# Optimization experiments

Measured on AMD Instinct MI355X. Metric: run time of the kernel, lower is better.

Reference implementation:

```python
import jax, jax.numpy as jnp
import numpy as np

N_NODES = 50000
N_EDGES = 800000
N_GRAPHS = 512
IN_DIM = 50
H = 128  # hidden_channels


def _init_linear(key, out_dim, in_dim, bias=True):
    k1, k2 = jax.random.split(key)
    bound = 1.0 / np.sqrt(in_dim)
    W = jax.random.uniform(k1, (out_dim, in_dim), jnp.float32, -bound, bound)
    if bias:
        b = jax.random.uniform(k2, (out_dim,), jnp.float32, -bound, bound)
        return W, b
    return W


def setup_inputs() -> dict:
    key = jax.random.key(0)
    ks = jax.random.split(key, 16)
    x = jax.random.normal(ks[0], (N_NODES, IN_DIM), jnp.float32)
    edge_index = jax.random.randint(ks[1], (2, N_EDGES), 0, N_NODES, jnp.int64)
    batch = jnp.sort(jax.random.randint(ks[2], (N_NODES,), 0, N_GRAPHS, jnp.int64))
    Wl1, bl1 = _init_linear(ks[3], H, IN_DIM)
    Wr1 = _init_linear(ks[4], H, IN_DIM, bias=False)
    Wl2, bl2 = _init_linear(ks[5], 2 * H, H)
    Wr2 = _init_linear(ks[6], 2 * H, H, bias=False)
    Wl3, bl3 = _init_linear(ks[7], 4 * H, 2 * H)
    Wr3 = _init_linear(ks[8], 4 * H, 2 * H, bias=False)
    Wf1, bf1 = _init_linear(ks[9], 2 * H, 4 * H)
    Wf2, bf2 = _init_linear(ks[10], H, 2 * H)
    Wo, bo = _init_linear(ks[11], 1, H)
    return dict(x=x, edge_index=edge_index, batch=batch,
                Wl1=Wl1, bl1=bl1, Wr1=Wr1,
                Wl2=Wl2, bl2=bl2, Wr2=Wr2,
                Wl3=Wl3, bl3=bl3, Wr3=Wr3,
                Wf1=Wf1, bf1=bf1, Wf2=Wf2, bf2=bf2, Wo=Wo, bo=bo)


def sage_conv(x, src, dst, deg_inv, Wl, bl, Wr):
    # mean-aggregate neighbor features at destination nodes, then linear
    agg = jax.ops.segment_sum(x[src], dst, num_segments=N_NODES) * deg_inv
    return agg @ Wl.T + bl + x @ Wr.T


def reference(x, edge_index, batch, Wl1, bl1, Wr1, Wl2, bl2, Wr2,
              Wl3, bl3, Wr3, Wf1, bf1, Wf2, bf2, Wo, bo):
    src, dst = edge_index[0], edge_index[1]
    deg = jax.ops.segment_sum(jnp.ones((N_EDGES,), x.dtype), dst, num_segments=N_NODES)
    deg_inv = (1.0 / jnp.maximum(deg, 1.0))[:, None]

    x1 = jax.nn.leaky_relu(sage_conv(x, src, dst, deg_inv, Wl1, bl1, Wr1))
    x2 = jax.nn.relu(sage_conv(x1, src, dst, deg_inv, Wl2, bl2, Wr2))
    x3 = jax.nn.relu(sage_conv(x2, src, dst, deg_inv, Wl3, bl3, Wr3))

    # global mean pool per graph
    pool_sum = jax.ops.segment_sum(x3, batch, num_segments=N_GRAPHS)
    cnt = jax.ops.segment_sum(jnp.ones((N_NODES,), x.dtype), batch, num_segments=N_GRAPHS)
    x_pool = pool_sum / jnp.maximum(cnt, 1.0)[:, None]

    x4 = jax.nn.relu(x_pool @ Wf1.T + bf1)
    x5 = jax.nn.relu(x4 @ Wf2.T + bf2)
    return jax.nn.sigmoid(x5 @ Wo.T + bo)
```

## Files before the change

### kernel.cpp

```cpp
#include <hip/hip_runtime.h>
#include <math.h>

#define N_NODES 50000
#define N_EDGES 800000
#define N_GRAPHS 512
#define M_PAD 50176
#define SEG_SZ 6250
#define EPT 8
#define SEG_BLOCKS 391
#define CAP 64

typedef unsigned char u8;
typedef unsigned short u16;
typedef unsigned int u32;
typedef long i64;
using floatx4 = __attribute__((ext_vector_type(4))) float;
using floatx2 = __attribute__((ext_vector_type(2))) float;

__device__ __forceinline__ u8 f2fp8(float v) {
    return (u8)(__builtin_amdgcn_cvt_pk_fp8_f32(v, v, 0, false) & 0xFF);
}
__device__ __forceinline__ u32 pack4fp8(float a, float b, float c, float d) {
    u32 p = __builtin_amdgcn_cvt_pk_fp8_f32(a, b, 0, false);
    return __builtin_amdgcn_cvt_pk_fp8_f32(c, d, p, true);
}
__device__ __forceinline__ void acc16fp8(float* acc, uint4 u) {
    const u32 w[4] = {u.x, u.y, u.z, u.w};
    #pragma unroll
    for (int j = 0; j < 4; ++j) {
        floatx2 lo = __builtin_amdgcn_cvt_pk_f32_fp8((int)w[j], false);
        floatx2 hi = __builtin_amdgcn_cvt_pk_f32_fp8((int)w[j], true);
        acc[j * 4 + 0] += lo[0]; acc[j * 4 + 1] += lo[1];
        acc[j * 4 + 2] += hi[0]; acc[j * 4 + 3] += hi[1];
    }
}

__device__ __forceinline__ void load_lds16(const u8* g, u8* l) {
    __builtin_amdgcn_global_load_lds(
        (const __attribute__((address_space(1))) u32*)g,
        (__attribute__((address_space(3))) u32*)l, 16, 0, 0);
}
template<int N> __device__ __forceinline__ void waitcnt_vm() {
    __builtin_amdgcn_s_waitcnt(0x0F70 | N);
}
__device__ __forceinline__ void raw_barrier() {
    asm volatile("s_barrier" ::: "memory");
}

__global__ __launch_bounds__(256) void prep_kernel(
    const int* __restrict__ batch, int* __restrict__ gstart,
    const float* __restrict__ x,
    const float* __restrict__ Wl1, const float* __restrict__ Wr1,
    const float* __restrict__ Wl2, const float* __restrict__ Wr2,
    const float* __restrict__ Wl3, const float* __restrict__ Wr3,
    const float* __restrict__ Wf1, const float* __restrict__ Wf2,
    u8* __restrict__ abuf1,
    u8* __restrict__ wb1, u8* __restrict__ wb2, u8* __restrict__ wb3,
    float* __restrict__ Wf1T, float* __restrict__ Wf2T)
{
    if (blockIdx.x < 196) {
        int i = blockIdx.x * 256 + threadIdx.x;
        if (i >= N_NODES) return;
        int b = batch[i];
        int bp = (i == 0) ? -1 : batch[i - 1];
        for (int g = bp + 1; g <= b; ++g) gstart[g] = i;
        if (i == N_NODES - 1)
            for (int g = b + 1; g <= N_GRAPHS; ++g) gstart[g] = N_NODES;
        return;
    }
    int i = (blockIdx.x - 196) * 256 + threadIdx.x;
    if (i < N_NODES * 16) {
        int n = i >> 4, c = (i & 15) * 4;
        float v[4];
        #pragma unroll
        for (int j = 0; j < 4; ++j) {
            int cc = c + j;
            v[j] = (cc < 50) ? x[n * 50 + cc] : 0.0f;
        }
        *(u32*)(abuf1 + (size_t)n * 128 + 64 + c) = pack4fp8(v[0], v[1], v[2], v[3]);
        return;
    }
    i -= N_NODES * 16;
    if (i < 128 * 64) {
        int o = i / 64, c = i % 64;
        float vl = (c < 50) ? Wl1[o * 50 + c] : 0.0f;
        float vr = (c < 50) ? Wr1[o * 50 + c] : 0.0f;
        wb1[(size_t)o * 128 + c] = f2fp8(vl);
        wb1[(size_t)o * 128 + 64 + c] = f2fp8(vr);
        return;
    }
    i -= 128 * 64;
    if (i < 256 * 128) {
        int o = i / 128, c = i % 128;
        wb2[(size_t)o * 256 + c] = f2fp8(Wl2[o * 128 + c]);
        wb2[(size_t)o * 256 + 128 + c] = f2fp8(Wr2[o * 128 + c]);
        return;
    }
    i -= 256 * 128;
    if (i < 512 * 256) {
        int o = i / 256, c = i % 256;
        wb3[(size_t)o * 512 + c] = f2fp8(Wl3[o * 256 + c]);
        wb3[(size_t)o * 512 + 256 + c] = f2fp8(Wr3[o * 256 + c]);
        return;
    }
    i -= 512 * 256;
    if (i < 256 * 512) {
        int o = i >> 9, k = i & 511;
        Wf1T[(size_t)k * 256 + o] = Wf1[(size_t)o * 512 + k];
        return;
    }
    i -= 256 * 512;
    if (i < 128 * 256) {
        int o = i >> 8, k = i & 255;
        Wf2T[(size_t)k * 128 + o] = Wf2[(size_t)o * 256 + k];
    }
}

__global__ __launch_bounds__(256) void fill_seg_kernel(const int* __restrict__ src,
                                                       const int* __restrict__ dst,
                                                       int* __restrict__ cursor,
                                                       u16* __restrict__ csr) {
    const int seg = blockIdx.x & 7;
    const int lo = seg * SEG_SZ, hi = lo + SEG_SZ;
    int e = (blockIdx.x >> 3) * (256 * EPT) + threadIdx.x;
    #pragma unroll
    for (int j = 0; j < EPT; ++j, e += 256) {
        if (e < N_EDGES) {
            int d = dst[e];
            if (d >= lo && d < hi) {
                int p = atomicAdd(&cursor[d], 1);
                csr[d * CAP + p] = (u16)src[e];
            }
        }
    }
}

template<int DINP>
__global__ __launch_bounds__(256) void csr_agg_kernel(const int* __restrict__ cnt,
                                                      const u16* __restrict__ csr,
                                                      u8* __restrict__ abuf) {
    constexpr int STRIDE = 2 * DINP;
    constexpr int LPR = DINP / 16;
    constexpr int EPW = 64 / LPR;
    const int wave = threadIdx.x >> 6, lane = threadIdx.x & 63;
    const int n = blockIdx.x * 4 + wave;
    if (n >= N_NODES) return;
    const int sub = lane / LPR;
    const int li = lane % LPR;
    const int deg = cnt[n];
    const int s0 = n * CAP, s1 = s0 + deg;

    float acc[16] = {};
    const u8* xin = abuf + DINP;

    int e = s0 + sub;
    for (; e + EPW < s1; e += 2 * EPW) {
        int i0 = csr[e], i1 = csr[e + EPW];
        uint4 u0 = *(const uint4*)(xin + (size_t)i0 * STRIDE + li * 16);
        uint4 u1 = *(const uint4*)(xin + (size_t)i1 * STRIDE + li * 16);
        acc16fp8(acc, u0);
        acc16fp8(acc, u1);
    }
    for (; e < s1; e += EPW) {
        int i0 = csr[e];
        uint4 u0 = *(const uint4*)(xin + (size_t)i0 * STRIDE + li * 16);
        acc16fp8(acc, u0);
    }

    #pragma unroll
    for (int off = 32; off >= LPR; off >>= 1) {
        #pragma unroll
        for (int c = 0; c < 16; ++c) acc[c] += __shfl_down(acc[c], off);
    }

    if (lane < LPR) {
        float sc = 1.0f / fmaxf((float)deg, 1.0f);
        uint4 o;
        o.x = pack4fp8(acc[0] * sc, acc[1] * sc, acc[2] * sc, acc[3] * sc);
        o.y = pack4fp8(acc[4] * sc, acc[5] * sc, acc[6] * sc, acc[7] * sc);
        o.z = pack4fp8(acc[8] * sc, acc[9] * sc, acc[10] * sc, acc[11] * sc);
        o.w = pack4fp8(acc[12] * sc, acc[13] * sc, acc[14] * sc, acc[15] * sc);
        *(uint4*)(abuf + (size_t)n * STRIDE + li * 16) = o;
    }
}

template<int K, int NB, int ACT>
__global__ __launch_bounds__(256) void gemm_fp8_kernel(
    const u8* __restrict__ A, const u8* __restrict__ W,
    const float* __restrict__ bias,
    u8* __restrict__ out8, int gstride, int goff, int N)
{
    constexpr int NKB = K / 32;
    constexpr int MT = M_PAD / 128;
    constexpr int MCHUNK = MT / 8;
    __shared__ __align__(16) u8 As[3][128 * 32];
    __shared__ __align__(16) u8 Bs[3][128 * 32];

    const int bx = blockIdx.x;
    const int xcd = bx & 7;
    const int seq = bx >> 3;
    const int n = seq % NB;
    const int m = xcd * MCHUNK + seq / NB;
    if (m >= MT) return;
    const int bm = m * 128;
    const int bn = n * 128;

    const int tid = threadIdx.x;
    const int wave = tid >> 6, lane = tid & 63;
    const int wm = (wave & 1) * 64, wn = (wave >> 1) * 64;
    const int lm = lane & 15, lq = lane >> 4;

    const int srow = wave * 32 + (lane >> 1);
    const int scol = ((lane & 1) ^ ((lane >> 3) & 1)) * 16;
    const u8* gA = A + (size_t)(bm + srow) * K + scol;
    const u8* gB = W + (size_t)(bn + srow) * K + scol;
    const int lbase = wave * 32 * 32;

    auto stage = [&](int s, int r) {
        const int ko = s * 32;
        load_lds16(gA + ko, &As[r][lbase]);
        load_lds16(gB + ko, &Bs[r][lbase]);
    };

    floatx4 acc[4][4] = {};

    stage(0, 0);
    stage(1, 1);

    const int csw = (((lq >> 1) ^ ((lm >> 2) & 1)) << 4) + (lq & 1) * 8;

    #pragma unroll
    for (int kb = 0; kb < NKB; ++kb) {
        if (kb + 2 < NKB) stage(kb + 2, (kb + 2) % 3);
        const int rem = NKB - 1 - kb;
        if (rem >= 2)      waitcnt_vm<4>();
        else if (rem == 1) waitcnt_vm<2>();
        else               waitcnt_vm<0>();
        raw_barrier();

        const int r = kb % 3;
        i64 af[4], bfr[4];
        #pragma unroll
        for (int mi = 0; mi < 4; ++mi)
            af[mi] = *(const i64*)&As[r][(wm + mi * 16 + lm) * 32 + csw];
        #pragma unroll
        for (int ni = 0; ni < 4; ++ni)
            bfr[ni] = *(const i64*)&Bs[r][(wn + ni * 16 + lm) * 32 + csw];
        #pragma unroll
        for (int mi = 0; mi < 4; ++mi)
            #pragma unroll
            for (int ni = 0; ni < 4; ++ni)
                acc[mi][ni] = __builtin_amdgcn_mfma_f32_16x16x32_fp8_fp8(
                    af[mi], bfr[ni], acc[mi][ni], 0, 0, 0);
        raw_barrier();
    }

    #pragma unroll
    for (int mi = 0; mi < 4; ++mi) {
        int node0 = bm + wm + mi * 16 + lq * 4;
        #pragma unroll
        for (int ni = 0; ni < 4; ++ni) {
            int o = bn + wn + ni * 16 + lm;
            float bi = bias[o];
            #pragma unroll
            for (int r = 0; r < 4; ++r) {
                int node = node0 + r;
                if (node >= N) continue;
                float v = acc[mi][ni][r] + bi;
                if (ACT == 0) v = (v > 0.0f) ? v : 0.01f * v;
                else          v = fmaxf(v, 0.0f);
                out8[(size_t)node * gstride + goff + o] = f2fp8(v);
            }
        }
    }
}

template<int K, int NB, int ACT>
__global__ __launch_bounds__(256) void gemm64_fp8_kernel(
    const u8* __restrict__ A, const u8* __restrict__ W,
    const float* __restrict__ bias,
    u8* __restrict__ out8, int gstride, int goff, int N)
{
    constexpr int NKB = K / 64;
    constexpr int MT = M_PAD / 128;
    constexpr int MCHUNK = MT / 8;
    __shared__ __align__(16) u8 As[3][128 * 64];
    __shared__ __align__(16) u8 Bs[3][128 * 64];

    const int bx = blockIdx.x;
    const int xcd = bx & 7;
    const int seq = bx >> 3;
    const int n = seq % NB;
    const int m = xcd * MCHUNK + seq / NB;
    if (m >= MT) return;
    const int bm = m * 128;
    const int bn = n * 128;

    const int tid = threadIdx.x;
    const int wave = tid >> 6, lane = tid & 63;
    const int wm = (wave & 1) * 64, wn = (wave >> 1) * 64;
    const int lm = lane & 15, lq = lane >> 4;

    const int srow = wave * 16 + (lane >> 2);
    const int scd  = ((lane & 3) ^ ((srow >> 1) & 3)) << 4;
    const u8* gA = A + (size_t)(bm + srow) * K + scd;
    const u8* gB = W + (size_t)(bn + srow) * K + scd;
    const int lbase = wave * 1024;

    auto stage = [&](int s, int r) {
        const int ko = s * 64;
        load_lds16(gA + ko,                    &As[r][lbase]);
        load_lds16(gA + (size_t)64 * K + ko,   &As[r][lbase + 4096]);
        load_lds16(gB + ko,                    &Bs[r][lbase]);
        load_lds16(gB + (size_t)64 * K + ko,   &Bs[r][lbase + 4096]);
    };

    floatx4 acc[4][4] = {};

    stage(0, 0);
    stage(1, 1);

    const int pr = (lm >> 1) & 3;
    const int c0 = (((lq >> 1) ^ pr) << 4)       + ((lq & 1) << 3);
    const int c1 = (((2 + (lq >> 1)) ^ pr) << 4) + ((lq & 1) << 3);

    #pragma unroll
    for (int kb = 0; kb < NKB; ++kb) {
        if (kb + 2 < NKB) stage(kb + 2, (kb + 2) % 3);
        const int rem = NKB - 1 - kb;
        if (rem >= 2)      waitcnt_vm<8>();
        else if (rem == 1) waitcnt_vm<4>();
        else               waitcnt_vm<0>();
        raw_barrier();

        const int r = kb % 3;
        i64 af[4][2], bfr[4][2];
        #pragma unroll
        for (int mi = 0; mi < 4; ++mi) {
            const int base = (wm + mi * 16 + lm) * 64;
            af[mi][0] = *(const i64*)&As[r][base + c0];
            af[mi][1] = *(const i64*)&As[r][base + c1];
        }
        #pragma unroll
        for (int ni = 0; ni < 4; ++ni) {
            const int base = (wn + ni * 16 + lm) * 64;
            bfr[ni][0] = *(const i64*)&Bs[r][base + c0];
            bfr[ni][1] = *(const i64*)&Bs[r][base + c1];
        }
        #pragma unroll
        for (int mi = 0; mi < 4; ++mi)
            #pragma unroll
            for (int ni = 0; ni < 4; ++ni) {
                acc[mi][ni] = __builtin_amdgcn_mfma_f32_16x16x32_fp8_fp8(
                    af[mi][0], bfr[ni][0], acc[mi][ni], 0, 0, 0);
                acc[mi][ni] = __builtin_amdgcn_mfma_f32_16x16x32_fp8_fp8(
                    af[mi][1], bfr[ni][1], acc[mi][ni], 0, 0, 0);
            }
        raw_barrier();
    }

    #pragma unroll
    for (int mi = 0; mi < 4; ++mi) {
        int node0 = bm + wm + mi * 16 + lq * 4;
        #pragma unroll
        for (int ni = 0; ni < 4; ++ni) {
            int o = bn + wn + ni * 16 + lm;
            float bi = bias[o];
            #pragma unroll
            for (int r = 0; r < 4; ++r) {
                int node = node0 + r;
                if (node >= N) continue;
                float v = acc[mi][ni][r] + bi;
                if (ACT == 0) v = (v > 0.0f) ? v : 0.01f * v;
                else          v = fmaxf(v, 0.0f);
                out8[(size_t)node * gstride + goff + o] = f2fp8(v);
            }
        }
    }
}

__global__ __launch_bounds__(256) void pool_kernel(
    const u8* __restrict__ x3, const int* __restrict__ gstart,
    float* __restrict__ pool)
{
    __shared__ float sacc[32][128];
    const int g = blockIdx.x >> 2;
    const int slab = blockIdx.x & 3;
    const int t = threadIdx.x;
    const int chain = t >> 3;
    const int li = t & 7;
    const int c0 = slab * 128 + li * 16;
    const int n0 = gstart[g], n1 = gstart[g + 1];

    float acc[16] = {};
    for (int n = n0 + chain; n < n1; n += 32) {
        uint4 u = *(const uint4*)(x3 + (size_t)n * 512 + c0);
        acc16fp8(acc, u);
    }
    #pragma unroll
    for (int j = 0; j < 16; ++j) sacc[chain][li * 16 + j] = acc[j];
    __syncthreads();
    if (t < 128) {
        float s = 0.0f;
        #pragma unroll
        for (int r = 0; r < 32; ++r) s += sacc[r][t];
        pool[(size_t)g * 512 + slab * 128 + t] = s;
    }
}

__global__ __launch_bounds__(256) void dense_head_kernel(
    const float* __restrict__ pool, const int* __restrict__ gstart,
    const float* __restrict__ Wf1T, const float* __restrict__ bf1,
    const float* __restrict__ Wf2T, const float* __restrict__ bf2,
    const float* __restrict__ Wo,  const float* __restrict__ bo,
    float* __restrict__ out)
{
    __shared__ float sp[512];
    __shared__ float s4[256];
    __shared__ float red[128];
    const int g = blockIdx.x;
    const int t = threadIdx.x;
    const float sc = 1.0f / fmaxf((float)(gstart[g + 1] - gstart[g]), 1.0f);

    sp[t]       = pool[(size_t)g * 512 + t] * sc;
    sp[t + 256] = pool[(size_t)g * 512 + 256 + t] * sc;
    __syncthreads();

    {
        float s = bf1[t];
        #pragma unroll 8
        for (int k = 0; k < 512; ++k) s += sp[k] * Wf1T[(size_t)k * 256 + t];
        s4[t] = fmaxf(s, 0.0f);
    }
    __syncthreads();
    if (t < 128) {
        float s = bf2[t];
        #pragma unroll 8
        for (int k = 0; k < 256; ++k) s += s4[k] * Wf2T[(size_t)k * 128 + t];
        red[t] = fmaxf(s, 0.0f) * Wo[t];
    }
    __syncthreads();
    for (int off = 64; off >= 1; off >>= 1) {
        if (t < off) red[t] += red[t + off];
        __syncthreads();
    }
    if (t == 0) out[g] = 1.0f / (1.0f + expf(-(red[0] + bo[0])));
}

extern "C" void kernel_launch(void* const* d_in, const int* in_sizes, int n_in,
                              void* d_out, int out_size, void* d_ws, size_t ws_size,
                              hipStream_t stream)
{
    const float* x     = (const float*)d_in[0];
    const int*   ei    = (const int*)  d_in[1];
    const int*   batch = (const int*)  d_in[2];
    const float* Wl1   = (const float*)d_in[3];
    const float* bl1   = (const float*)d_in[4];
    const float* Wr1   = (const float*)d_in[5];
    const float* Wl2   = (const float*)d_in[6];
    const float* bl2   = (const float*)d_in[7];
    const float* Wr2   = (const float*)d_in[8];
    const float* Wl3   = (const float*)d_in[9];
    const float* bl3   = (const float*)d_in[10];
    const float* Wr3   = (const float*)d_in[11];
    const float* Wf1   = (const float*)d_in[12];
    const float* bf1   = (const float*)d_in[13];
    const float* Wf2   = (const float*)d_in[14];
    const float* bf2   = (const float*)d_in[15];
    const float* Wo    = (const float*)d_in[16];
    const float* bo    = (const float*)d_in[17];

    const int* src = ei;
    const int* dst = ei + N_EDGES;

    char* p = (char*)d_ws;
    auto alloc = [&](size_t bytes) { char* r = p; p += (bytes + 255) & ~(size_t)255; return r; };
    int*   gstart = (int*)  alloc(513 * 4);
    float* pool   = (float*)alloc((size_t)512 * 512 * 4);
    float* Wf1T   = (float*)alloc((size_t)512 * 256 * 4);
    float* Wf2T   = (float*)alloc((size_t)256 * 128 * 4);
    u8*    abuf1  = (u8*)   alloc((size_t)M_PAD * 128);
    u8*    abuf2  = (u8*)   alloc((size_t)M_PAD * 256);
    u8*    abuf3  = (u8*)   alloc((size_t)M_PAD * 512);
    u8*    x3buf8 = (u8*)   alloc((size_t)M_PAD * 512);
    u8*    wb1    = (u8*)   alloc((size_t)128 * 128);
    u8*    wb2    = (u8*)   alloc((size_t)256 * 256);
    u8*    wb3    = (u8*)   alloc((size_t)512 * 512);
    int*   cursor = (int*)  alloc(50176 * 4);
    u16*   csr    = (u16*)  alloc((size_t)50176 * CAP * 2);

    hipMemsetAsync(cursor, 0, 50176 * 4, stream);
    const int CONV_N = N_NODES * 16 + 128 * 64 + 256 * 128 + 512 * 256
                     + 256 * 512 + 128 * 256;
    const int CONV_BLOCKS = (CONV_N + 255) / 256;
    prep_kernel<<<196 + CONV_BLOCKS, 256, 0, stream>>>(
        batch, gstart, x, Wl1, Wr1, Wl2, Wr2, Wl3, Wr3, Wf1, Wf2,
        abuf1, wb1, wb2, wb3, Wf1T, Wf2T);
    fill_seg_kernel<<<SEG_BLOCKS * 8, 256, 0, stream>>>(src, dst, cursor, csr);

    const int GB = 12500;
    const int GEMM_GRID = 49 * 8;

    csr_agg_kernel<64><<<GB, 256, 0, stream>>>(cursor, csr, abuf1);
    gemm_fp8_kernel<128, 1, 0><<<GEMM_GRID * 1, 256, 0, stream>>>(
        abuf1, wb1, bl1, abuf2, 256, 128, N_NODES);

    csr_agg_kernel<128><<<GB, 256, 0, stream>>>(cursor, csr, abuf2);
    gemm64_fp8_kernel<256, 2, 1><<<GEMM_GRID * 2, 256, 0, stream>>>(
        abuf2, wb2, bl2, abuf3, 512, 256, N_NODES);

    csr_agg_kernel<256><<<GB, 256, 0, stream>>>(cursor, csr, abuf3);
    gemm64_fp8_kernel<512, 4, 1><<<GEMM_GRID * 4, 256, 0, stream>>>(
        abuf3, wb3, bl3, x3buf8, 512, 0, N_NODES);

    pool_kernel<<<N_GRAPHS * 4, 256, 0, stream>>>(x3buf8, gstart, pool);
    dense_head_kernel<<<N_GRAPHS, 256, 0, stream>>>(
        pool, gstart, Wf1T, bf1, Wf2T, bf2, Wo, bo, (float*)d_out);
}
```

Baseline: 339.1 us.

## Fuse CSR fill into prep kernel, pack fp8 accumulation, batch dense head

Moves the edge-bucketing CSR fill into the prep kernel's grid, removing one kernel launch. The fp8 accumulation loops in the aggregation and pool kernels now add into two-wide float vectors, so the compiler can use packed float adds. The dense head now handles four graphs per block and reuses each weight load across them, cutting weight traffic by four but launching only 128 blocks. The fused prep kernel depends on the transposed weights (Wf1T/Wf2T) being read only by the later dense head, so merging the fill with the conversions adds no ordering problem.

```diff
diff --git a/kernel.cpp b/kernel.cpp
--- a/kernel.cpp
+++ b/kernel.cpp
@@ -8,6 +8,7 @@
 #define SEG_SZ 6250
 #define EPT 8
 #define SEG_BLOCKS 391
+#define FILL_BLOCKS (SEG_BLOCKS * 8)
 #define CAP 64
 
 typedef unsigned char u8;
@@ -24,14 +25,12 @@
     u32 p = __builtin_amdgcn_cvt_pk_fp8_f32(a, b, 0, false);
     return __builtin_amdgcn_cvt_pk_fp8_f32(c, d, p, true);
 }
-__device__ __forceinline__ void acc16fp8(float* acc, uint4 u) {
+__device__ __forceinline__ void acc16fp8p(floatx2* acc2, uint4 u) {
     const u32 w[4] = {u.x, u.y, u.z, u.w};
     #pragma unroll
     for (int j = 0; j < 4; ++j) {
-        floatx2 lo = __builtin_amdgcn_cvt_pk_f32_fp8((int)w[j], false);
-        floatx2 hi = __builtin_amdgcn_cvt_pk_f32_fp8((int)w[j], true);
-        acc[j * 4 + 0] += lo[0]; acc[j * 4 + 1] += lo[1];
-        acc[j * 4 + 2] += hi[0]; acc[j * 4 + 3] += hi[1];
+        acc2[j * 2 + 0] += __builtin_amdgcn_cvt_pk_f32_fp8((int)w[j], false);
+        acc2[j * 2 + 1] += __builtin_amdgcn_cvt_pk_f32_fp8((int)w[j], true);
     }
 }
 
@@ -48,6 +47,8 @@
 }
 
 __global__ __launch_bounds__(256) void prep_kernel(
+    const int* __restrict__ src, const int* __restrict__ dst,
+    int* __restrict__ cursor, u16* __restrict__ csr,
     const int* __restrict__ batch, int* __restrict__ gstart,
     const float* __restrict__ x,
     const float* __restrict__ Wl1, const float* __restrict__ Wr1,
@@ -58,8 +59,25 @@
     u8* __restrict__ wb1, u8* __restrict__ wb2, u8* __restrict__ wb3,
     float* __restrict__ Wf1T, float* __restrict__ Wf2T)
 {
-    if (blockIdx.x < 196) {
-        int i = blockIdx.x * 256 + threadIdx.x;
+    if (blockIdx.x < FILL_BLOCKS) {
+        const int seg = blockIdx.x & 7;
+        const int lo = seg * SEG_SZ, hi = lo + SEG_SZ;
+        int e = (blockIdx.x >> 3) * (256 * EPT) + threadIdx.x;
+        #pragma unroll
+        for (int j = 0; j < EPT; ++j, e += 256) {
+            if (e < N_EDGES) {
+                int d = dst[e];
+                if (d >= lo && d < hi) {
+                    int p = atomicAdd(&cursor[d], 1);
+                    csr[d * CAP + p] = (u16)src[e];
+                }
+            }
+        }
+        return;
+    }
+    const int bx = blockIdx.x - FILL_BLOCKS;
+    if (bx < 196) {
+        int i = bx * 256 + threadIdx.x;
         if (i >= N_NODES) return;
         int b = batch[i];
         int bp = (i == 0) ? -1 : batch[i - 1];
@@ -68,7 +86,7 @@
             for (int g = b + 1; g <= N_GRAPHS; ++g) gstart[g] = N_NODES;
         return;
     }
-    int i = (blockIdx.x - 196) * 256 + threadIdx.x;
+    int i = (bx - 196) * 256 + threadIdx.x;
     if (i < N_NODES * 16) {
         int n = i >> 4, c = (i & 15) * 4;
         float v[4];
@@ -113,25 +131,6 @@
     if (i < 128 * 256) {
         int o = i >> 8, k = i & 255;
         Wf2T[(size_t)k * 128 + o] = Wf2[(size_t)o * 256 + k];
-    }
-}
-
-__global__ __launch_bounds__(256) void fill_seg_kernel(const int* __restrict__ src,
-                                                       const int* __restrict__ dst,
-                                                       int* __restrict__ cursor,
-                                                       u16* __restrict__ csr) {
-    const int seg = blockIdx.x & 7;
-    const int lo = seg * SEG_SZ, hi = lo + SEG_SZ;
-    int e = (blockIdx.x >> 3) * (256 * EPT) + threadIdx.x;
-    #pragma unroll
-    for (int j = 0; j < EPT; ++j, e += 256) {
-        if (e < N_EDGES) {
-            int d = dst[e];
-            if (d >= lo && d < hi) {
-                int p = atomicAdd(&cursor[d], 1);
-                csr[d * CAP + p] = (u16)src[e];
-            }
-        }
     }
 }
 
@@ -150,7 +149,7 @@
     const int deg = cnt[n];
     const int s0 = n * CAP, s1 = s0 + deg;
 
-    float acc[16] = {};
+    floatx2 acc2[8] = {};
     const u8* xin = abuf + DINP;
 
     int e = s0 + sub;
@@ -158,28 +157,33 @@
         int i0 = csr[e], i1 = csr[e + EPW];
         uint4 u0 = *(const uint4*)(xin + (size_t)i0 * STRIDE + li * 16);
         uint4 u1 = *(const uint4*)(xin + (size_t)i1 * STRIDE + li * 16);
-        acc16fp8(acc, u0);
-        acc16fp8(acc, u1);
+        acc16fp8p(acc2, u0);
+        acc16fp8p(acc2, u1);
     }
     for (; e < s1; e += EPW) {
         int i0 = csr[e];
         uint4 u0 = *(const uint4*)(xin + (size_t)i0 * STRIDE + li * 16);
-        acc16fp8(acc, u0);
+        acc16fp8p(acc2, u0);
     }
 
     #pragma unroll
     for (int off = 32; off >= LPR; off >>= 1) {
         #pragma unroll
-        for (int c = 0; c < 16; ++c) acc[c] += __shfl_down(acc[c], off);
+        for (int c = 0; c < 8; ++c) {
+            floatx2 o;
+            o[0] = __shfl_down(acc2[c][0], off);
+            o[1] = __shfl_down(acc2[c][1], off);
+            acc2[c] += o;
+        }
     }
 
     if (lane < LPR) {
         float sc = 1.0f / fmaxf((float)deg, 1.0f);
         uint4 o;
-        o.x = pack4fp8(acc[0] * sc, acc[1] * sc, acc[2] * sc, acc[3] * sc);
-        o.y = pack4fp8(acc[4] * sc, acc[5] * sc, acc[6] * sc, acc[7] * sc);
-        o.z = pack4fp8(acc[8] * sc, acc[9] * sc, acc[10] * sc, acc[11] * sc);
-        o.w = pack4fp8(acc[12] * sc, acc[13] * sc, acc[14] * sc, acc[15] * sc);
+        o.x = pack4fp8(acc2[0][0] * sc, acc2[0][1] * sc, acc2[1][0] * sc, acc2[1][1] * sc);
+        o.y = pack4fp8(acc2[2][0] * sc, acc2[2][1] * sc, acc2[3][0] * sc, acc2[3][1] * sc);
+        o.z = pack4fp8(acc2[4][0] * sc, acc2[4][1] * sc, acc2[5][0] * sc, acc2[5][1] * sc);
+        o.w = pack4fp8(acc2[6][0] * sc, acc2[6][1] * sc, acc2[7][0] * sc, acc2[7][1] * sc);
         *(uint4*)(abuf + (size_t)n * STRIDE + li * 16) = o;
     }
 }
@@ -392,13 +396,16 @@
     const int c0 = slab * 128 + li * 16;
     const int n0 = gstart[g], n1 = gstart[g + 1];
 
-    float acc[16] = {};
+    floatx2 acc2[8] = {};
     for (int n = n0 + chain; n < n1; n += 32) {
         uint4 u = *(const uint4*)(x3 + (size_t)n * 512 + c0);
-        acc16fp8(acc, u);
-    }
-    #pragma unroll
-    for (int j = 0; j < 16; ++j) sacc[chain][li * 16 + j] = acc[j];
+        acc16fp8p(acc2, u);
+    }
+    #pragma unroll
+    for (int c = 0; c < 8; ++c) {
+        sacc[chain][li * 16 + c * 2 + 0] = acc2[c][0];
+        sacc[chain][li * 16 + c * 2 + 1] = acc2[c][1];
+    }
     __syncthreads();
     if (t < 128) {
         float s = 0.0f;
@@ -415,36 +422,57 @@
     const float* __restrict__ Wo,  const float* __restrict__ bo,
     float* __restrict__ out)
 {
-    __shared__ float sp[512];
-    __shared__ float s4[256];
-    __shared__ float red[128];
-    const int g = blockIdx.x;
+    __shared__ float sp[4][512];
+    __shared__ float s4[4][256];
+    __shared__ float red[128][4];
+    const int g0 = blockIdx.x * 4;
     const int t = threadIdx.x;
-    const float sc = 1.0f / fmaxf((float)(gstart[g + 1] - gstart[g]), 1.0f);
-
-    sp[t]       = pool[(size_t)g * 512 + t] * sc;
-    sp[t + 256] = pool[(size_t)g * 512 + 256 + t] * sc;
+
+    #pragma unroll
+    for (int g = 0; g < 4; ++g) {
+        float sc = 1.0f / fmaxf((float)(gstart[g0 + g + 1] - gstart[g0 + g]), 1.0f);
+        sp[g][t]       = pool[(size_t)(g0 + g) * 512 + t] * sc;
+        sp[g][t + 256] = pool[(size_t)(g0 + g) * 512 + 256 + t] * sc;
+    }
     __syncthreads();
 
     {
-        float s = bf1[t];
+        float s[4];
+        #pragma unroll
+        for (int g = 0; g < 4; ++g) s[g] = bf1[t];
         #pragma unroll 8
-        for (int k = 0; k < 512; ++k) s += sp[k] * Wf1T[(size_t)k * 256 + t];
-        s4[t] = fmaxf(s, 0.0f);
+        for (int k = 0; k < 512; ++k) {
+            float w = Wf1T[(size_t)k * 256 + t];
+            #pragma unroll
+            for (int g = 0; g < 4; ++g) s[g] += sp[g][k] * w;
+        }
+        #pragma unroll
+        for (int g = 0; g < 4; ++g) s4[g][t] = fmaxf(s[g], 0.0f);
     }
     __syncthreads();
     if (t < 128) {
-        float s = bf2[t];
+        float s[4];
+        #pragma unroll
+        for (int g = 0; g < 4; ++g) s[g] = bf2[t];
         #pragma unroll 8
-        for (int k = 0; k < 256; ++k) s += s4[k] * Wf2T[(size_t)k * 128 + t];
-        red[t] = fmaxf(s, 0.0f) * Wo[t];
+        for (int k = 0; k < 256; ++k) {
+            float w = Wf2T[(size_t)k * 128 + t];
+            #pragma unroll
+            for (int g = 0; g < 4; ++g) s[g] += s4[g][k] * w;
+        }
+        float wo = Wo[t];
+        #pragma unroll
+        for (int g = 0; g < 4; ++g) red[t][g] = fmaxf(s[g], 0.0f) * wo;
     }
     __syncthreads();
     for (int off = 64; off >= 1; off >>= 1) {
-        if (t < off) red[t] += red[t + off];
+        if (t < off) {
+            #pragma unroll
+            for (int g = 0; g < 4; ++g) red[t][g] += red[t + off][g];
+        }
         __syncthreads();
     }
-    if (t == 0) out[g] = 1.0f / (1.0f + expf(-(red[0] + bo[0])));
+    if (t < 4) out[g0 + t] = 1.0f / (1.0f + expf(-(red[0][t] + bo[0])));
 }
 
 extern "C" void kernel_launch(void* const* d_in, const int* in_sizes, int n_in,
@@ -493,10 +521,10 @@
     const int CONV_N = N_NODES * 16 + 128 * 64 + 256 * 128 + 512 * 256
                      + 256 * 512 + 128 * 256;
     const int CONV_BLOCKS = (CONV_N + 255) / 256;
-    prep_kernel<<<196 + CONV_BLOCKS, 256, 0, stream>>>(
+    prep_kernel<<<FILL_BLOCKS + 196 + CONV_BLOCKS, 256, 0, stream>>>(
+        src, dst, cursor, csr,
         batch, gstart, x, Wl1, Wr1, Wl2, Wr2, Wl3, Wr3, Wf1, Wf2,
         abuf1, wb1, wb2, wb3, Wf1T, Wf2T);
-    fill_seg_kernel<<<SEG_BLOCKS * 8, 256, 0, stream>>>(src, dst, cursor, csr);
 
     const int GB = 12500;
     const int GEMM_GRID = 49 * 8;
@@ -514,6 +542,6 @@
         abuf3, wb3, bl3, x3buf8, 512, 0, N_NODES);
 
     pool_kernel<<<N_GRAPHS * 4, 256, 0, stream>>>(x3buf8, gstart, pool);
-    dense_head_kernel<<<N_GRAPHS, 256, 0, stream>>>(
+    dense_head_kernel<<<N_GRAPHS / 4, 256, 0, stream>>>(
         pool, gstart, Wf1T, bf1, Wf2T, bf2, Wo, bo, (float*)d_out);
 }
```

Result: no change. 334.4 us (median of 2 runs) (-1.4%).
